# Performance work log

Hardware: AMD Instinct MI355X
Metric: run time of the kernel (lower is better)

## Reference

```python
import jax, jax.numpy as jnp
import numpy as np

N, E = 50000, 800000
IN, H, D, C = 128, 4, 32, 40   # in_feats, heads, num_hiddens, n_classes
SLOPE, EPS = 0.2, 1e-5


def _glorot(key, shape, fan_in):
    return jax.random.normal(key, shape, dtype=jnp.float32) * (1.0 / np.sqrt(fan_in))


def setup_inputs() -> dict:
    key = jax.random.key(0)
    ks = jax.random.split(key, 24)
    inp = {
        "feat": jax.random.normal(ks[0], (N, IN), dtype=jnp.float32),
        "src": jax.random.randint(ks[1], (E,), 0, N, dtype=jnp.int32),
        "dst": jax.random.randint(ks[2], (E,), 0, N, dtype=jnp.int32),
    }
    # layer dims: (in_hidden, out_hidden)
    dims = [(IN, D), (H * D, D), (H * D, C)]
    k = 3
    for i, (fin, fout) in enumerate(dims):
        inp[f"Wc{i}"] = _glorot(ks[k], (fin, H * fout), fin); k += 1
        inp[f"al{i}"] = _glorot(ks[k], (H, fout), fout); k += 1
        inp[f"ar{i}"] = _glorot(ks[k], (H, fout), fout); k += 1
        inp[f"bc{i}"] = jnp.zeros((H * fout,), dtype=jnp.float32)
        inp[f"Wl{i}"] = _glorot(ks[k], (fin, H * fout), fin); k += 1
    for i in range(2):  # BN after layers 0 and 1
        inp[f"g{i}"] = jnp.ones((H * D,), dtype=jnp.float32)
        inp[f"b{i}"] = jnp.zeros((H * D,), dtype=jnp.float32)
    inp["bias_last"] = jnp.zeros((C,), dtype=jnp.float32)
    return inp


def _gat_layer(x, src, dst, Wc, al, ar, bc, Wl):
    n = x.shape[0]
    h, d = al.shape
    z = (x @ Wc).reshape(n, h, d)                      # [N,H,D]
    el = jnp.sum(z * al, axis=-1)                      # [N,H]
    er = jnp.sum(z * ar, axis=-1)                      # [N,H]
    e = jax.nn.leaky_relu(el[src] + er[dst], SLOPE)    # [E,H]
    m = jax.ops.segment_max(e, dst, num_segments=n)    # edge-softmax (stable)
    ex = jnp.exp(e - m[dst])
    s = jax.ops.segment_sum(ex, dst, num_segments=n)
    alpha = ex / jnp.where(s == 0, 1.0, s)[dst]        # [E,H]
    agg = jax.ops.segment_sum(alpha[:, :, None] * z[src], dst, num_segments=n)
    conv = agg + bc.reshape(h, d)
    lin = (x @ Wl).reshape(n, h, d)
    return conv + lin                                   # [N,H,D]


def _bn(x, g, b):
    mu = jnp.mean(x, axis=0)
    var = jnp.mean((x - mu) ** 2, axis=0)
    return (x - mu) * jax.lax.rsqrt(var + EPS) * g + b


def reference(feat, src, dst,
              Wc0, al0, ar0, bc0, Wl0,
              Wc1, al1, ar1, bc1, Wl1,
              Wc2, al2, ar2, bc2, Wl2,
              g0, b0, g1, b1, bias_last):
    h = feat
    h = _gat_layer(h, src, dst, Wc0, al0, ar0, bc0, Wl0)
    h = jax.nn.relu(_bn(h.reshape(h.shape[0], -1), g0, b0))
    h = _gat_layer(h, src, dst, Wc1, al1, ar1, bc1, Wl1)
    h = jax.nn.relu(_bn(h.reshape(h.shape[0], -1), g1, b1))
    h = _gat_layer(h, src, dst, Wc2, al2, ar2, bc2, Wl2)
    h = h.mean(axis=1)                                  # mean over heads -> [N,C]
    return h + bias_last
```

## Files before the change

kernel.cpp:

```cpp
#include <hip/hip_runtime.h>
#include <hip/hip_bf16.h>

typedef __hip_bfloat16 bf16;
typedef __attribute__((ext_vector_type(8))) short short8;
typedef __attribute__((ext_vector_type(4))) float f32x4;

__device__ __forceinline__ float b2f(bf16 x) { return __bfloat162float(x); }
__device__ __forceinline__ float bits2f(unsigned short u) {
    return __uint_as_float(((unsigned)u) << 16);
}
__device__ __forceinline__ float ldw(const void* p, int i, int m) {
    return m ? ((const float*)p)[i] : b2f(((const bf16*)p)[i]);
}

__global__ __launch_bounds__(256) void k_zero_probe(int* __restrict__ counts, float* __restrict__ bn0,
                                                    float* __restrict__ bn1, int n,
                                                    const void* __restrict__ feat, int* __restrict__ mode) {
    int t = blockIdx.x * 256 + threadIdx.x;
    if (t < n) counts[t] = 0;
    if (t < 256) { bn0[t] = 0.f; bn1[t] = 0.f; }
    if (blockIdx.x == 0 && threadIdx.x < 64) {
        const bf16* p = (const bf16*)feat;
        int lane = threadIdx.x;
        float m = 0.f;
        for (int i = lane; i < 2048; i += 64) {
            float v = fabsf(b2f(p[2 * i]));
            if (!(v < 1e30f)) v = 1e30f;
            m = fmaxf(m, v);
        }
        #pragma unroll
        for (int off = 32; off > 0; off >>= 1) m = fmaxf(m, __shfl_xor(m, off, 64));
        if (lane == 0) *mode = (m > 1e8f) ? 1 : 0;
    }
}

struct SmallDesc { const void* src; float* dst; int n; };
struct SmallArgs { SmallDesc d[14]; };
__global__ __launch_bounds__(256) void k_prep(const void* __restrict__ Wc0, const void* __restrict__ Wl0,
                                              const void* __restrict__ Wc1, const void* __restrict__ Wl1,
                                              const void* __restrict__ Wc2, const void* __restrict__ Wl2,
                                              bf16* __restrict__ Wt0, bf16* __restrict__ Wt1,
                                              bf16* __restrict__ Wt2, SmallArgs sa,
                                              const int* __restrict__ mode) {
    int m = *mode;
    int bx = blockIdx.x;
    if (bx < 416) {
        int t = bx * 256 + threadIdx.x;
        const void* Wc; const void* Wl; bf16* Wt; int HC;
        if (t < 32768)       { Wc = Wc0; Wl = Wl0; Wt = Wt0; HC = 128; }
        else if (t < 65536)  { t -= 32768; Wc = Wc1; Wl = Wl1; Wt = Wt1; HC = 128; }
        else                 { t -= 65536; Wc = Wc2; Wl = Wl2; Wt = Wt2; HC = 160; }
        int k = t & 127, c = t >> 7;
        float v = (c < HC) ? ldw(Wc, k * HC + c, m) : ldw(Wl, k * HC + c - HC, m);
        int tile = c >> 4, c16 = c & 15, kg = k >> 5, q = (k >> 3) & 3, j = k & 7;
        Wt[tile * 2048 + kg * 512 + c16 * 32 + q * 8 + j] = __float2bfloat16(v);
    } else {
        #pragma unroll 1
        for (int i = 0; i < 14; i++) {
            const SmallDesc sd = sa.d[i];
            for (int t = threadIdx.x; t < sd.n; t += 256) sd.dst[t] = ldw(sd.src, t, m);
        }
    }
}


__global__ __launch_bounds__(256) void k_hist(const int* __restrict__ dst, int* __restrict__ counts, int e) {
    int t = blockIdx.x * 256 + threadIdx.x;
    if (t < e) atomicAdd(&counts[dst[t]], 1);
}

__global__ __launch_bounds__(1024) void k_scan(const int* __restrict__ counts, int* __restrict__ row_ptr,
                                               int* __restrict__ cursor, int n) {
    __shared__ int wsum[16];
    __shared__ int carry_s;
    int lane = threadIdx.x & 63, w = threadIdx.x >> 6;
    if (threadIdx.x == 0) carry_s = 0;
    __syncthreads();
    for (int base = 0; base < n; base += 4096) {
        int i0 = base + (int)threadIdx.x * 4;
        int4 v = {0, 0, 0, 0};
        if (i0 + 3 < n) v = *(const int4*)(counts + i0);
        else if (i0 < n) {
            v.x = counts[i0];
            if (i0 + 1 < n) v.y = counts[i0 + 1];
            if (i0 + 2 < n) v.z = counts[i0 + 2];
        }
        int t1 = v.x + v.y, t2 = t1 + v.z, t3 = t2 + v.w;
        int x = t3;
        #pragma unroll
        for (int off = 1; off < 64; off <<= 1) {
            int t = __shfl_up(x, off, 64);
            if (lane >= off) x += t;
        }
        if (lane == 63) wsum[w] = x;
        __syncthreads();
        if (w == 0 && lane < 16) {
            int s = wsum[lane];
            #pragma unroll
            for (int off = 1; off < 16; off <<= 1) {
                int t = __shfl_up(s, off, 64);
                if (lane >= off) s += t;
            }
            wsum[lane] = s;
        }
        __syncthreads();
        int carry = carry_s;
        int woff = (w == 0) ? 0 : wsum[w - 1];
        int e0 = carry + woff + x - t3;
        if (i0 + 3 < n) {
            int4 rp = {e0, e0 + v.x, e0 + t1, e0 + t2};
            *(int4*)(row_ptr + i0) = rp;
            *(int4*)(cursor + i0) = rp;
        } else if (i0 < n) {
            row_ptr[i0] = e0; cursor[i0] = e0;
            if (i0 + 1 < n) { row_ptr[i0 + 1] = e0 + v.x; cursor[i0 + 1] = e0 + v.x; }
            if (i0 + 2 < n) { row_ptr[i0 + 2] = e0 + t1; cursor[i0 + 2] = e0 + t1; }
        }
        __syncthreads();
        if (threadIdx.x == 0) carry_s = carry + wsum[15];
        __syncthreads();
    }
    if (threadIdx.x == 0) row_ptr[n] = carry_s;
}

__global__ __launch_bounds__(256) void k_scatter(const int* __restrict__ src, const int* __restrict__ dst,
                                                 int* __restrict__ cursor, int* __restrict__ ssrc,
                                                 int e, int rpb) {
    int range = blockIdx.x & 7;
    int t = (blockIdx.x >> 3) * 256 + threadIdx.x;
    if (t < e) {
        int d = dst[t];
        if ((int)((unsigned)d / (unsigned)rpb) == range) {
            int idx = atomicAdd(&cursor[d], 1);
            ssrc[idx] = src[t];
        }
    }
}

template <int HC, int CT, int AMODE, bool FELR>
__global__ __launch_bounds__(256) void k_gemm_mfma(const void* __restrict__ Av, const int* __restrict__ mode,
                                                   const bf16* __restrict__ Wt,
                                                   bf16* __restrict__ Zh, float* __restrict__ Lin,
                                                   const float* __restrict__ alp, const float* __restrict__ arp,
                                                   float* __restrict__ elp, float* __restrict__ erp,
                                                   const float* __restrict__ bnsum, const float* __restrict__ bnsq,
                                                   const float* __restrict__ gg, const float* __restrict__ bb,
                                                   float invn, int n) {
    __shared__ short lds_a[64 * 136];
    __shared__ float lds_bn[256];
    int tid = threadIdx.x;
    int wv = tid >> 6, lane = tid & 63;
    int quad = lane >> 4, m16 = lane & 15;
    int row0 = blockIdx.x * 64 + wv * 16;
    int row0b = blockIdx.x * 64;
    int col0 = blockIdx.y * (CT * 16);
    if constexpr (AMODE == 2) {
        if (tid < 128) {
            float mu = bnsum[tid] * invn;
            float var = bnsq[tid] * invn - mu * mu;
            float sc = rsqrtf(var + 1e-5f) * gg[tid];
            lds_bn[tid] = sc;
            lds_bn[128 + tid] = bb[tid] - mu * sc;
        }
        __syncthreads();
    }
    bool af32 = false;
    if constexpr (AMODE == 1) af32 = (*mode != 0);
    #pragma unroll
    for (int i = 0; i < 4; i++) {
        int f = i * 256 + tid;
        int row = f >> 4, c8 = f & 15;
        int arow = row0b + row; if (arow >= n) arow = n - 1;
        union { bf16 h[8]; short8 s; } u;
        if (AMODE == 2 || (AMODE == 1 && af32)) {
            const float4* ap = (const float4*)((const float*)Av + (size_t)arow * 128 + c8 * 8);
            float4 g0v = ap[0], g1v = ap[1];
            float vals[8] = {g0v.x, g0v.y, g0v.z, g0v.w, g1v.x, g1v.y, g1v.z, g1v.w};
            if constexpr (AMODE == 2) {
                int c0 = c8 * 8;
                #pragma unroll
                for (int j = 0; j < 8; j++) {
                    float r = vals[j] * lds_bn[c0 + j] + lds_bn[128 + c0 + j];
                    vals[j] = r > 0.f ? r : 0.f;
                }
            }
            #pragma unroll
            for (int j = 0; j < 8; j++) u.h[j] = __float2bfloat16(vals[j]);
        } else {
            u.s = *(const short8*)((const bf16*)Av + (size_t)arow * 128 + c8 * 8);
        }
        *(short8*)(&lds_a[row * 136 + c8 * 8]) = u.s;
    }
    __syncthreads();
    f32x4 acc[CT] = {};
    const short8* Bp = (const short8*)Wt;
    int lr = wv * 16 + m16;
    int ctb = blockIdx.y * CT;
    #pragma unroll
    for (int k8 = 0; k8 < 16; k8 += 4) {
        short8 a = *(const short8*)(&lds_a[lr * 136 + (k8 + quad) * 8]);
        #pragma unroll
        for (int c = 0; c < CT; c++) {
            short8 b = Bp[(size_t)(ctb + c) * 256 + k8 * 16 + m16 * 4 + quad];
            acc[c] = __builtin_amdgcn_mfma_f32_16x16x32_bf16(a, b, acc[c], 0, 0, 0);
        }
    }
    if constexpr (FELR && HC == 128) {
        if (blockIdx.y == 0) {
            float a0[4], a1[4], r0[4], r1[4];
            #pragma unroll
            for (int h = 0; h < 4; h++) {
                a0[h] = alp[h * 32 + m16]; a1[h] = alp[h * 32 + 16 + m16];
                r0[h] = arp[h * 32 + m16]; r1[h] = arp[h * 32 + 16 + m16];
            }
            #pragma unroll
            for (int reg = 0; reg < 4; reg++) {
                float eh[8];
                #pragma unroll
                for (int h = 0; h < 4; h++) {
                    eh[h]     = acc[2 * h][reg] * a0[h] + acc[2 * h + 1][reg] * a1[h];
                    eh[4 + h] = acc[2 * h][reg] * r0[h] + acc[2 * h + 1][reg] * r1[h];
                }
                #pragma unroll
                for (int off = 1; off < 16; off <<= 1) {
                    #pragma unroll
                    for (int k = 0; k < 8; k++) eh[k] += __shfl_xor(eh[k], off, 64);
                }
                int r = row0 + quad * 4 + reg;
                float vl = (m16 & 2) ? ((m16 & 1) ? eh[3] : eh[2]) : ((m16 & 1) ? eh[1] : eh[0]);
                float vr = (m16 & 2) ? ((m16 & 1) ? eh[7] : eh[6]) : ((m16 & 1) ? eh[5] : eh[4]);
                if (r < n && m16 < 4) { elp[(size_t)r * 4 + m16] = vl; erp[(size_t)r * 4 + m16] = vr; }
            }
        }
    }
    if constexpr (FELR && HC == 160) {
        if (blockIdx.y == 0) {
            float alv[10], arv[10];
            #pragma unroll
            for (int c = 0; c < 10; c++) { alv[c] = alp[c * 16 + m16]; arv[c] = arp[c * 16 + m16]; }
            #pragma unroll
            for (int reg = 0; reg < 4; reg++) {
                float eh[8] = {0.f, 0.f, 0.f, 0.f, 0.f, 0.f, 0.f, 0.f};
                #pragma unroll
                for (int c = 0; c < 10; c++) {
                    int col = c * 16 + m16;
                    float zl = acc[c][reg] * alv[c];
                    float zr = acc[c][reg] * arv[c];
                    bool h0 = col < 40, h1 = (col >= 40) & (col < 80);
                    bool h2 = (col >= 80) & (col < 120), h3 = col >= 120;
                    eh[0] += h0 ? zl : 0.f; eh[1] += h1 ? zl : 0.f;
                    eh[2] += h2 ? zl : 0.f; eh[3] += h3 ? zl : 0.f;
                    eh[4] += h0 ? zr : 0.f; eh[5] += h1 ? zr : 0.f;
                    eh[6] += h2 ? zr : 0.f; eh[7] += h3 ? zr : 0.f;
                }
                #pragma unroll
                for (int off = 1; off < 16; off <<= 1) {
                    #pragma unroll
                    for (int k = 0; k < 8; k++) eh[k] += __shfl_xor(eh[k], off, 64);
                }
                int r = row0 + quad * 4 + reg;
                float vl = (m16 & 2) ? ((m16 & 1) ? eh[3] : eh[2]) : ((m16 & 1) ? eh[1] : eh[0]);
                float vr = (m16 & 2) ? ((m16 & 1) ? eh[7] : eh[6]) : ((m16 & 1) ? eh[5] : eh[4]);
                if (r < n && m16 < 4) { elp[(size_t)r * 4 + m16] = vl; erp[(size_t)r * 4 + m16] = vr; }
            }
        }
    }
    #pragma unroll
    for (int c = 0; c < CT; c++) {
        int gc = col0 + c * 16 + m16;
        #pragma unroll
        for (int reg = 0; reg < 4; reg++) {
            int r = row0 + quad * 4 + reg;
            if (r >= n) continue;
            float v = acc[c][reg];
            if (gc < HC) Zh[(size_t)r * HC + gc] = __float2bfloat16(v);
            else         Lin[(size_t)r * HC + gc - HC] = v;
        }
    }
}

template <int HC, int D, bool LAST>
__global__ __launch_bounds__(256, 8) void k_gather(const int* __restrict__ row_ptr, const int* __restrict__ ssrc,
                                                   const float* __restrict__ el, const float* __restrict__ er,
                                                   const float* __restrict__ bc, const bf16* __restrict__ Z,
                                                   float* __restrict__ Y, const float* __restrict__ bias,
                                                   float* __restrict__ out, int n) {
    constexpr int DPL = HC / 16;
    constexpr int UN = (DPL == 8) ? 4 : 2;
    int node = (int)((blockIdx.x * blockDim.x + threadIdx.x) >> 6);
    int lane = threadIdx.x & 63;
    if (node >= n) return;
    int qi = lane >> 4;
    int t16 = lane & 15;
    int hq = t16 >> 2;
    int beg = row_ptr[node], end = row_ptr[node + 1];
    float4 er4 = ((const float4*)er)[node];
    const float4* el4p = (const float4*)el;
    const bf16* Zt = Z + t16 * DPL;
    float acc[DPL];
    #pragma unroll
    for (int k = 0; k < DPL; k++) acc[k] = 0.f;
    float ss = 0.f;
    for (int base = beg; base < end; base += 64) {
        int idx = base + lane;
        bool valid = idx < end;
        int s_my = valid ? ssrc[idx] : 0;
        float4 e4 = el4p[s_my];
        float x0 = e4.x + er4.x; x0 = x0 > 0.f ? x0 : 0.2f * x0;
        float x1 = e4.y + er4.y; x1 = x1 > 0.f ? x1 : 0.2f * x1;
        float x2 = e4.z + er4.z; x2 = x2 > 0.f ? x2 : 0.2f * x2;
        float x3 = e4.w + er4.w; x3 = x3 > 0.f ? x3 : 0.2f * x3;
        float w0 = valid ? __expf(x0) : 0.f;
        float w1 = valid ? __expf(x1) : 0.f;
        float w2 = valid ? __expf(x2) : 0.f;
        float w3 = valid ? __expf(x3) : 0.f;
        int cnt = end - base; if (cnt > 64) cnt = 64;
        int iters = (cnt + 3) >> 2;
        for (int j = 0; j < iters; j += UN) {
            int sv[UN]; float gv[UN];
            #pragma unroll
            for (int f = 0; f < UN; f++) {
                int sl = qi + ((j + f) << 2);
                sv[f] = __shfl(s_my, sl, 64);
                float a0 = __shfl(w0, sl, 64);
                float a1 = __shfl(w1, sl, 64);
                float a2 = __shfl(w2, sl, 64);
                float a3 = __shfl(w3, sl, 64);
                gv[f] = (hq & 2) ? ((hq & 1) ? a3 : a2) : ((hq & 1) ? a1 : a0);
                ss += gv[f];
            }
            if constexpr (DPL == 8) {
                short8 z[UN];
                #pragma unroll
                for (int f = 0; f < UN; f++) z[f] = *(const short8*)(Zt + (size_t)sv[f] * HC);
                #pragma unroll
                for (int f = 0; f < UN; f++) {
                    #pragma unroll
                    for (int k = 0; k < 8; k++)
                        acc[k] += gv[f] * bits2f((unsigned short)z[f][k]);
                }
            } else {
                __hip_bfloat162 z[UN][DPL / 2];
                #pragma unroll
                for (int f = 0; f < UN; f++) {
                    const __hip_bfloat162* z2 = (const __hip_bfloat162*)(Zt + (size_t)sv[f] * HC);
                    #pragma unroll
                    for (int k2 = 0; k2 < DPL / 2; k2++) z[f][k2] = z2[k2];
                }
                #pragma unroll
                for (int f = 0; f < UN; f++) {
                    #pragma unroll
                    for (int k2 = 0; k2 < DPL / 2; k2++) {
                        acc[2 * k2]     += gv[f] * b2f(z[f][k2].x);
                        acc[2 * k2 + 1] += gv[f] * b2f(z[f][k2].y);
                    }
                }
            }
        }
    }
    #pragma unroll
    for (int k = 0; k < DPL; k++) {
        acc[k] += __shfl_xor(acc[k], 16, 64);
        acc[k] += __shfl_xor(acc[k], 32, 64);
    }
    ss += __shfl_xor(ss, 16, 64);
    ss += __shfl_xor(ss, 32, 64);
    float inv = (end > beg) ? 1.f / ss : 0.f;
    if constexpr (!LAST) {
        if ((lane & 48) == 0) {
            float* yr = Y + (size_t)node * HC + t16 * DPL;
            const float* bcr = bc + t16 * DPL;
            #pragma unroll
            for (int k = 0; k < DPL; k++) yr[k] += acc[k] * inv + bcr[k];
        }
    } else {
        float yv[DPL];
        const float* lr = Y + (size_t)node * HC + t16 * DPL;
        const float* bcr = bc + t16 * DPL;
        #pragma unroll
        for (int k = 0; k < DPL; k++) yv[k] = acc[k] * inv + bcr[k] + lr[k];
        #pragma unroll
        for (int k = 0; k < DPL; k++) {
            yv[k] += __shfl_xor(yv[k], 4, 64);
            yv[k] += __shfl_xor(yv[k], 8, 64);
        }
        if (lane < 4) {
            float* orow = out + (size_t)node * 40 + t16 * DPL;
            const float* br = bias + t16 * DPL;
            #pragma unroll
            for (int k = 0; k < DPL; k++) orow[k] = 0.25f * yv[k] + br[k];
        }
    }
}

__global__ __launch_bounds__(256) void k_bn_stats(const float* __restrict__ Y, float* __restrict__ sum,
                                                  float* __restrict__ sumsq, int n) {
    __shared__ float4 lds_s[8][32];
    __shared__ float4 lds_q[8][32];
    int t = threadIdx.x;
    int q = t & 31, g = t >> 5;
    const float4* Y4 = (const float4*)Y;
    float4 s = {0.f, 0.f, 0.f, 0.f}, ss = {0.f, 0.f, 0.f, 0.f};
    const int stride = 128 * 8;
    int r = blockIdx.x * 8 + g;
    for (; r + stride < n; r += 2 * stride) {
        float4 v0 = Y4[(size_t)r * 32 + q];
        float4 v1 = Y4[(size_t)(r + stride) * 32 + q];
        s.x += v0.x; s.y += v0.y; s.z += v0.z; s.w += v0.w;
        ss.x += v0.x * v0.x; ss.y += v0.y * v0.y; ss.z += v0.z * v0.z; ss.w += v0.w * v0.w;
        s.x += v1.x; s.y += v1.y; s.z += v1.z; s.w += v1.w;
        ss.x += v1.x * v1.x; ss.y += v1.y * v1.y; ss.z += v1.z * v1.z; ss.w += v1.w * v1.w;
    }
    if (r < n) {
        float4 v = Y4[(size_t)r * 32 + q];
        s.x += v.x; s.y += v.y; s.z += v.z; s.w += v.w;
        ss.x += v.x * v.x; ss.y += v.y * v.y; ss.z += v.z * v.z; ss.w += v.w * v.w;
    }
    lds_s[g][q] = s; lds_q[g][q] = ss;
    __syncthreads();
    if (t < 32) {
        float4 S = lds_s[0][t], Q = lds_q[0][t];
        #pragma unroll
        for (int g2 = 1; g2 < 8; g2++) {
            float4 a = lds_s[g2][t], b = lds_q[g2][t];
            S.x += a.x; S.y += a.y; S.z += a.z; S.w += a.w;
            Q.x += b.x; Q.y += b.y; Q.z += b.z; Q.w += b.w;
        }
        atomicAdd(&sum[4 * t + 0], S.x); atomicAdd(&sum[4 * t + 1], S.y);
        atomicAdd(&sum[4 * t + 2], S.z); atomicAdd(&sum[4 * t + 3], S.w);
        atomicAdd(&sumsq[4 * t + 0], Q.x); atomicAdd(&sumsq[4 * t + 1], Q.y);
        atomicAdd(&sumsq[4 * t + 2], Q.z); atomicAdd(&sumsq[4 * t + 3], Q.w);
    }
}


extern "C" void kernel_launch(void* const* d_in, const int* in_sizes, int n_in,
                              void* d_out, int out_size, void* d_ws, size_t ws_size,
                              hipStream_t stream) {
    (void)n_in; (void)out_size; (void)ws_size;
    const int N = in_sizes[0] / 128;
    const int E = in_sizes[1];

    const int* src = (const int*)d_in[1];
    const int* dst = (const int*)d_in[2];
    float* out = (float*)d_out;

    char* p = (char*)d_ws;
    auto carve = [&](size_t bytes) {
        void* q = (void*)p;
        p += (bytes + 255) & ~(size_t)255;
        return q;
    };
    int*   mode    = (int*)  carve(256);
    bf16*  zh      = (bf16*) carve((size_t)N * 160 * 2);
    float* P0      = (float*)carve((size_t)N * 160 * 4);
    float* P1      = (float*)carve((size_t)N * 128 * 4);
    float* el      = (float*)carve((size_t)N * 4 * 4);
    float* er      = (float*)carve((size_t)N * 4 * 4);
    float* bn0     = (float*)carve(256 * 4);
    float* bn1     = (float*)carve(256 * 4);
    int*   counts  = (int*)  carve((size_t)N * 4);
    int*   row_ptr = (int*)  carve((size_t)(N + 1) * 4);
    int*   cursor  = (int*)  carve((size_t)N * 4);
    int*   ssrc    = (int*)  carve((size_t)E * 4);
    bf16*  Wt0     = (bf16*) carve((size_t)2 * 128 * 128 * 2);
    bf16*  Wt1     = (bf16*) carve((size_t)2 * 128 * 128 * 2);
    bf16*  Wt2     = (bf16*) carve((size_t)2 * 160 * 128 * 2);
    const int small_idx[14] = {4, 5, 6, 9, 10, 11, 14, 15, 16, 18, 19, 20, 21, 22};
    float* Wsm[14];
    for (int j = 0; j < 14; j++) Wsm[j] = (float*)carve((size_t)in_sizes[small_idx[j]] * 4);

    const float* alw[3] = {Wsm[0], Wsm[3], Wsm[6]};
    const float* arw[3] = {Wsm[1], Wsm[4], Wsm[7]};
    const float* bcw[3] = {Wsm[2], Wsm[5], Wsm[8]};
    const float* g0 = Wsm[9];
    const float* b0 = Wsm[10];
    const float* g1 = Wsm[11];
    const float* b1 = Wsm[12];
    const float* bias_last = Wsm[13];

    const int EB = (E + 255) / 256;
    const int GB_ROWS = (N + 63) / 64;
    const int NODE_BLK = (N + 3) / 4;
    const float invn = 1.f / (float)N;
    const int RPB = (N + 7) / 8;

    k_zero_probe<<<(N + 255) / 256, 256, 0, stream>>>(counts, bn0, bn1, N, d_in[0], mode);
    SmallArgs sa;
    for (int j = 0; j < 14; j++) sa.d[j] = SmallDesc{d_in[small_idx[j]], Wsm[j], in_sizes[small_idx[j]]};
    k_prep<<<417, 256, 0, stream>>>(d_in[3], d_in[7], d_in[8], d_in[12], d_in[13], d_in[17],
                                    Wt0, Wt1, Wt2, sa, mode);
    k_hist<<<EB, 256, 0, stream>>>(dst, counts, E);
    k_scan<<<1, 1024, 0, stream>>>(counts, row_ptr, cursor, N);
    k_scatter<<<8 * EB, 256, 0, stream>>>(src, dst, cursor, ssrc, E, RPB);

    k_gemm_mfma<128, 8, 1, true><<<dim3(GB_ROWS, 2), 256, 0, stream>>>(
        d_in[0], mode, Wt0, zh, P0, alw[0], arw[0], el, er,
        nullptr, nullptr, nullptr, nullptr, 0.f, N);
    k_gather<128, 32, false><<<NODE_BLK, 256, 0, stream>>>(row_ptr, ssrc, el, er, bcw[0], zh,
                                                           P0, nullptr, nullptr, N);
    k_bn_stats<<<128, 256, 0, stream>>>(P0, bn0, bn0 + 128, N);

    k_gemm_mfma<128, 8, 2, true><<<dim3(GB_ROWS, 2), 256, 0, stream>>>(
        P0, mode, Wt1, zh, P1, alw[1], arw[1], el, er,
        bn0, bn0 + 128, g0, b0, invn, N);
    k_gather<128, 32, false><<<NODE_BLK, 256, 0, stream>>>(row_ptr, ssrc, el, er, bcw[1], zh,
                                                           P1, nullptr, nullptr, N);
    k_bn_stats<<<128, 256, 0, stream>>>(P1, bn1, bn1 + 128, N);

    k_gemm_mfma<160, 10, 2, true><<<dim3(GB_ROWS, 2), 256, 0, stream>>>(
        P1, mode, Wt2, zh, P0, alw[2], arw[2], el, er,
        bn1, bn1 + 128, g1, b1, invn, N);
    k_gather<160, 40, true><<<NODE_BLK, 256, 0, stream>>>(row_ptr, ssrc, el, er, bcw[2], zh,
                                                          P0, bias_last, out, N);
}
```

Baseline: 467.3 us.

## Partition histogram atomics by dst range, widen scan per thread, coalesce weight prep

```diff
diff --git a/kernel.cpp b/kernel.cpp
--- a/kernel.cpp
+++ b/kernel.cpp
@@ -46,13 +46,12 @@
     int bx = blockIdx.x;
     if (bx < 416) {
         int t = bx * 256 + threadIdx.x;
-        const void* Wc; const void* Wl; bf16* Wt; int HC;
-        if (t < 32768)       { Wc = Wc0; Wl = Wl0; Wt = Wt0; HC = 128; }
-        else if (t < 65536)  { t -= 32768; Wc = Wc1; Wl = Wl1; Wt = Wt1; HC = 128; }
-        else                 { t -= 65536; Wc = Wc2; Wl = Wl2; Wt = Wt2; HC = 160; }
-        int k = t & 127, c = t >> 7;
-        float v = (c < HC) ? ldw(Wc, k * HC + c, m) : ldw(Wl, k * HC + c - HC, m);
-        int tile = c >> 4, c16 = c & 15, kg = k >> 5, q = (k >> 3) & 3, j = k & 7;
+        const void* Wc; const void* Wl; bf16* Wt; int HC, c2, k;
+        if (t < 32768)       { Wc = Wc0; Wl = Wl0; Wt = Wt0; HC = 128; c2 = t & 255; k = t >> 8; }
+        else if (t < 65536)  { t -= 32768; Wc = Wc1; Wl = Wl1; Wt = Wt1; HC = 128; c2 = t & 255; k = t >> 8; }
+        else                 { t -= 65536; Wc = Wc2; Wl = Wl2; Wt = Wt2; HC = 160; c2 = t % 320; k = t / 320; }
+        float v = (c2 < HC) ? ldw(Wc, k * HC + c2, m) : ldw(Wl, k * HC + c2 - HC, m);
+        int tile = c2 >> 4, c16 = c2 & 15, kg = k >> 5, q = (k >> 3) & 3, j = k & 7;
         Wt[tile * 2048 + kg * 512 + c16 * 32 + q * 8 + j] = __float2bfloat16(v);
     } else {
         #pragma unroll 1
@@ -64,9 +63,14 @@
 }
 
 
-__global__ __launch_bounds__(256) void k_hist(const int* __restrict__ dst, int* __restrict__ counts, int e) {
-    int t = blockIdx.x * 256 + threadIdx.x;
-    if (t < e) atomicAdd(&counts[dst[t]], 1);
+__global__ __launch_bounds__(256) void k_hist(const int* __restrict__ dst, int* __restrict__ counts,
+                                              int e, int rpb) {
+    int range = blockIdx.x & 7;
+    int t = (blockIdx.x >> 3) * 256 + threadIdx.x;
+    if (t < e) {
+        int d = dst[t];
+        if ((int)((unsigned)d / (unsigned)rpb) == range) atomicAdd(&counts[d], 1);
+    }
 }
 
 __global__ __launch_bounds__(1024) void k_scan(const int* __restrict__ counts, int* __restrict__ row_ptr,
@@ -76,17 +80,24 @@
     int lane = threadIdx.x & 63, w = threadIdx.x >> 6;
     if (threadIdx.x == 0) carry_s = 0;
     __syncthreads();
-    for (int base = 0; base < n; base += 4096) {
-        int i0 = base + (int)threadIdx.x * 4;
-        int4 v = {0, 0, 0, 0};
-        if (i0 + 3 < n) v = *(const int4*)(counts + i0);
-        else if (i0 < n) {
-            v.x = counts[i0];
-            if (i0 + 1 < n) v.y = counts[i0 + 1];
-            if (i0 + 2 < n) v.z = counts[i0 + 2];
-        }
-        int t1 = v.x + v.y, t2 = t1 + v.z, t3 = t2 + v.w;
-        int x = t3;
+    for (int base = 0; base < n; base += 16384) {
+        int i0 = base + (int)threadIdx.x * 16;
+        int v[16];
+        #pragma unroll
+        for (int jb = 0; jb < 16; jb += 4) {
+            int idx = i0 + jb;
+            if (idx + 3 < n) {
+                int4 t4 = *(const int4*)(counts + idx);
+                v[jb] = t4.x; v[jb + 1] = t4.y; v[jb + 2] = t4.z; v[jb + 3] = t4.w;
+            } else {
+                #pragma unroll
+                for (int q = 0; q < 4; q++) v[jb + q] = (idx + q < n) ? counts[idx + q] : 0;
+            }
+        }
+        int pre[16]; int tot = 0;
+        #pragma unroll
+        for (int j = 0; j < 16; j++) { pre[j] = tot; tot += v[j]; }
+        int x = tot;
         #pragma unroll
         for (int off = 1; off < 64; off <<= 1) {
             int t = __shfl_up(x, off, 64);
@@ -106,15 +117,19 @@
         __syncthreads();
         int carry = carry_s;
         int woff = (w == 0) ? 0 : wsum[w - 1];
-        int e0 = carry + woff + x - t3;
-        if (i0 + 3 < n) {
-            int4 rp = {e0, e0 + v.x, e0 + t1, e0 + t2};
-            *(int4*)(row_ptr + i0) = rp;
-            *(int4*)(cursor + i0) = rp;
-        } else if (i0 < n) {
-            row_ptr[i0] = e0; cursor[i0] = e0;
-            if (i0 + 1 < n) { row_ptr[i0 + 1] = e0 + v.x; cursor[i0 + 1] = e0 + v.x; }
-            if (i0 + 2 < n) { row_ptr[i0 + 2] = e0 + t1; cursor[i0 + 2] = e0 + t1; }
+        int excl = carry + woff + x - tot;
+        #pragma unroll
+        for (int jb = 0; jb < 16; jb += 4) {
+            int idx = i0 + jb;
+            if (idx + 3 < n) {
+                int4 rp = {excl + pre[jb], excl + pre[jb + 1], excl + pre[jb + 2], excl + pre[jb + 3]};
+                *(int4*)(row_ptr + idx) = rp;
+                *(int4*)(cursor + idx) = rp;
+            } else {
+                #pragma unroll
+                for (int q = 0; q < 4; q++)
+                    if (idx + q < n) { row_ptr[idx + q] = excl + pre[jb + q]; cursor[idx + q] = excl + pre[jb + q]; }
+            }
         }
         __syncthreads();
         if (threadIdx.x == 0) carry_s = carry + wsum[15];
@@ -490,7 +505,7 @@
     for (int j = 0; j < 14; j++) sa.d[j] = SmallDesc{d_in[small_idx[j]], Wsm[j], in_sizes[small_idx[j]]};
     k_prep<<<417, 256, 0, stream>>>(d_in[3], d_in[7], d_in[8], d_in[12], d_in[13], d_in[17],
                                     Wt0, Wt1, Wt2, sa, mode);
-    k_hist<<<EB, 256, 0, stream>>>(dst, counts, E);
+    k_hist<<<8 * EB, 256, 0, stream>>>(dst, counts, E, RPB);
     k_scan<<<1, 1024, 0, stream>>>(counts, row_ptr, cursor, N);
     k_scatter<<<8 * EB, 256, 0, stream>>>(src, dst, cursor, ssrc, E, RPB);
 
```

After: 468.6 us. Within noise of the previous version (+0.3%).
